# Optimization experiments

Hardware: AMD Instinct MI355X
Metric: run time of the kernel (lower is better)

Reference implementation:

```python
import jax, jax.numpy as jnp
import numpy as np

N, D_IN, D, E, B = 30000, 512, 512, 300000, 4096
N_RES, N_DNN = 2, 2
EPS = 1e-5


def _ln(x, g, b):
    mu = jnp.mean(x, axis=-1, keepdims=True)
    var = jnp.mean((x - mu) ** 2, axis=-1, keepdims=True)
    return (x - mu) * jax.lax.rsqrt(var + EPS) * g + b


def setup_inputs() -> dict:
    key = jax.random.key(0)
    ks = jax.random.split(key, 16)
    s = 1.0 / np.sqrt(D)
    inp = {
        "node_feat": jax.random.normal(ks[0], (N, D_IN), jnp.float32),
        "edge_hop0": jax.random.randint(ks[1], (2, E), 0, N, jnp.int32),
        "edge_hop1": jax.random.randint(ks[2], (2, E), 0, N, jnp.int32),
        "target_idx": jax.random.randint(ks[3], (B,), 0, N, jnp.int32),
        # node transform
        "Wt": jax.random.normal(ks[4], (D_IN, D), jnp.float32) / np.sqrt(D_IN),
        "bt": jnp.zeros((D,), jnp.float32),
        # GATConv (shared across both hops, one relation)
        "Wf": jax.random.normal(ks[5], (D, D), jnp.float32) * s,
        "bf": jnp.zeros((D,), jnp.float32),
        "w_att": jax.random.normal(ks[6], (2 * D,), jnp.float32) * s,
        "b_att": jnp.zeros((), jnp.float32),
        "gat_bias": jnp.zeros((D,), jnp.float32),
        # Res_DNN
        "Wp": jax.random.normal(ks[7], (D, D), jnp.float32) * s,
        "bp": jnp.zeros((D,), jnp.float32),
        "dnn_W": jax.random.normal(ks[8], (N_RES, N_DNN, D, D), jnp.float32) * s,
        "dnn_b": jnp.zeros((N_RES, N_DNN, D), jnp.float32),
        "dnn_g": jnp.ones((N_RES, N_DNN, D), jnp.float32),
        "dnn_beta": jnp.zeros((N_RES, N_DNN, D), jnp.float32),
        "res_g": jnp.ones((N_RES, D), jnp.float32),
        "res_beta": jnp.zeros((N_RES, D), jnp.float32),
        "Wc": jax.random.normal(ks[9], (D, 1), jnp.float32) * s,
        "bc": jnp.zeros((1,), jnp.float32),
    }
    return inp


def _gat(feat, edges, Wf, bf, w_att, b_att, gat_bias):
    # dst and src are the same node set / same features here
    h = feat @ Wf + bf                      # [N, D]
    di, si = edges[0], edges[1]             # [E], [E]
    # att(concat(dst_h, src_h)) == dst_h @ w[:D] + src_h @ w[D:] + b
    sd = h @ w_att[:D]                      # [N]
    ss = h @ w_att[D:]                      # [N]
    e = jnp.tanh(sd[di] + ss[si] + b_att)   # [E]
    # sparse softmax per destination row
    m = jax.ops.segment_max(e, di, num_segments=N)
    a = jnp.exp(e - m[di])
    denom = jax.ops.segment_sum(a, di, num_segments=N)
    alpha = a / denom[di]                   # [E]
    # sparse-mm aggregation
    out = jax.ops.segment_sum(alpha[:, None] * h[si], di, num_segments=N)
    return out + gat_bias


def reference(node_feat, edge_hop0, edge_hop1, target_idx, Wt, bt, Wf, bf,
              w_att, b_att, gat_bias, Wp, bp, dnn_W, dnn_b, dnn_g, dnn_beta,
              res_g, res_beta, Wc, bc):
    # node-type feature transform (dropout is identity at inference)
    feat = node_feat @ Wt + bt              # [N, D]
    # hops processed from last to first: hop1 then hop0
    for edges in (edge_hop1, edge_hop0):
        g = _gat(feat, edges, Wf, bf, w_att, b_att, gat_bias)
        feat = (feat + g) * 0.5             # mean of stacked [orig, gat_out]
    h = feat[target_idx]                    # [B, D]
    # Res_DNN head
    h = h @ Wp + bp
    for r in range(N_RES):
        sc = h
        for i in range(N_DNN):
            h = _ln(jnp.tanh(h @ dnn_W[r, i] + dnn_b[r, i]), dnn_g[r, i], dnn_beta[r, i])
        h = _ln(jnp.tanh(sc + h), res_g[r], res_beta[r])
    logits = h @ Wc + bc                    # [B, 1]
    return jax.nn.sigmoid(logits)
```

## Files before the change

### kernel.cpp

```cpp
#include <hip/hip_runtime.h>

#define D 512
typedef unsigned short ushort_t;
typedef __attribute__((ext_vector_type(8))) short bf16x8;
typedef __attribute__((ext_vector_type(4))) short bf16x4;
typedef __attribute__((ext_vector_type(4))) float f32x4;

static __device__ __forceinline__ ushort_t f2bf(float f) {
  unsigned u = __float_as_uint(f);
  u += 0x7fffu + ((u >> 16) & 1u);
  return (ushort_t)(u >> 16);
}
static __device__ __forceinline__ float bf2f(ushort_t h) {
  return __uint_as_float(((unsigned)h) << 16);
}

static __device__ __forceinline__ void gld_lds16(const void* g, void* lds) {
  __builtin_amdgcn_global_load_lds(
      (const __attribute__((address_space(1))) unsigned int*)g,
      (__attribute__((address_space(3))) unsigned int*)lds, 16, 0, 0);
}

__global__ __launch_bounds__(256) void pack_weight(
    const float* __restrict__ W, ushort_t* __restrict__ out, int K, int N, int nmat) {
  int i = blockIdx.x * 256 + threadIdx.x;
  const int per = K * N;
  if (i >= per * nmat) return;
  const int mat = i / per;
  const int r = i - mat * per;
  const int k = r / N, n = r - k * N;
  const int nt = n >> 4, col = n & 15, kt = k >> 5, kg = (k >> 3) & 3, j = k & 7;
  out[(size_t)mat * per + (((size_t)nt * (K >> 5) + kt) << 9) + ((kg << 4) + col) * 8 + j] =
      f2bf(W[(size_t)mat * per + r]);
}

__global__ __launch_bounds__(256) void conv_bf16_pad(
    const float* __restrict__ in, ushort_t* __restrict__ out, int M, int Mp, int K) {
  const size_t i4 = ((size_t)blockIdx.x * 256 + threadIdx.x) * 4;
  if (i4 >= (size_t)Mp * K) return;
  const int row = (int)(i4 / K);
  ushort4 o;
  if (row < M) {
    const float4 v = *reinterpret_cast<const float4*>(&in[i4]);
    o.x = f2bf(v.x); o.y = f2bf(v.y); o.z = f2bf(v.z); o.w = f2bf(v.w);
  } else {
    o.x = o.y = o.z = o.w = 0;
  }
  *reinterpret_cast<ushort4*>(&out[i4]) = o;
}

__global__ __launch_bounds__(512) void gemm_mfma(
    const ushort_t* __restrict__ A, const ushort_t* __restrict__ Bp,
    const float* __restrict__ bias, ushort_t* __restrict__ C16, int N, int K) {
  __shared__ __align__(16) ushort_t As[2][8 * 512];
  __shared__ __align__(16) ushort_t Bs[2][8 * 512];
  const int nwg = gridDim.x;
  const int q = nwg >> 3, rm = nwg & 7;
  const int xcd = blockIdx.x & 7, kk = blockIdx.x >> 3;
  const int lin = (xcd < rm ? xcd * (q + 1) : rm * (q + 1) + (xcd - rm) * q) + kk;
  const int m0 = (lin >> 2) * 128;
  const int n0 = (lin & 3) * 128;
  const int tid = threadIdx.x;
  const int lane = tid & 63;
  const int wid = tid >> 6;
  const int wm = wid >> 1;
  const int wn = wid & 1;
  const int arow = lane & 15;
  const int akoff = (lane >> 4) * 8;
  const int kt32 = K >> 5;
  f32x4 acc[2][4] = {};

  auto stage = [&](int kt, int b) {
    const int k0 = kt * 32;
    gld_lds16(&A[(size_t)(m0 + wid * 16 + arow) * K + k0 + akoff],
              &As[b][wid * 512]);
    gld_lds16(&Bp[(((size_t)(n0 / 16 + wid) * kt32 + kt) << 9) + lane * 8],
              &Bs[b][wid * 512]);
  };

  stage(0, 0);
  __syncthreads();
  int cur = 0;
  for (int t = 0; t < kt32; ++t) {
    if (t + 1 < kt32) stage(t + 1, cur ^ 1);
    bf16x8 af[2], bfr[4];
#pragma unroll
    for (int mi = 0; mi < 2; ++mi)
      af[mi] = *reinterpret_cast<const bf16x8*>(&As[cur][(wm * 2 + mi) * 512 + lane * 8]);
#pragma unroll
    for (int ni = 0; ni < 4; ++ni)
      bfr[ni] = *reinterpret_cast<const bf16x8*>(&Bs[cur][(wn * 4 + ni) * 512 + lane * 8]);
#pragma unroll
    for (int mi = 0; mi < 2; ++mi)
#pragma unroll
      for (int ni = 0; ni < 4; ++ni)
        acc[mi][ni] = __builtin_amdgcn_mfma_f32_16x16x32_bf16(af[mi], bfr[ni], acc[mi][ni], 0, 0, 0);
    __syncthreads();
    cur ^= 1;
  }
#pragma unroll
  for (int mi = 0; mi < 2; ++mi) {
    const int row = m0 + wm * 32 + mi * 16 + ((lane >> 4) << 2);
#pragma unroll
    for (int ni = 0; ni < 4; ++ni) {
      const int col = n0 + wn * 64 + ni * 16 + (lane & 15);
      const float bv = bias[col];
#pragma unroll
      for (int r = 0; r < 4; ++r)
        C16[(size_t)(row + r) * N + col] = f2bf(acc[mi][ni][r] + bv);
    }
  }
}

__global__ __launch_bounds__(256) void rowdot2_w(
    const ushort_t* __restrict__ hb, const float* __restrict__ w_att,
    float* __restrict__ sd, float* __restrict__ ss, int Nn) {
  const int r = blockIdx.x * 4 + (threadIdx.x >> 6);
  const int lane = threadIdx.x & 63;
  if (r >= Nn) return;
  const bf16x8 hv = *reinterpret_cast<const bf16x8*>(&hb[(size_t)r * D + lane * 8]);
  float d0 = 0.f, d1 = 0.f;
#pragma unroll
  for (int q = 0; q < 8; ++q) {
    const float v = bf2f((ushort_t)hv[q]);
    d0 += v * w_att[lane * 8 + q];
    d1 += v * w_att[D + lane * 8 + q];
  }
#pragma unroll
  for (int off = 32; off > 0; off >>= 1) {
    d0 += __shfl_xor(d0, off);
    d1 += __shfl_xor(d1, off);
  }
  if (lane == 0) { sd[r] = d0; ss[r] = d1; }
}

__global__ void fill_bucket(const int* __restrict__ e1, const int* __restrict__ e0,
                            int* __restrict__ cnt, int* __restrict__ bucket,
                            int Nn, int E) {
  const int e = blockIdx.x * blockDim.x + threadIdx.x;
  if (e >= E) return;
  const int d1 = e1[e];
  const int p1 = atomicAdd(&cnt[d1], 1);
  if (p1 < 64) bucket[(size_t)d1 * 64 + p1] = e1[E + e];
  const int d0 = e0[e];
  const int p0 = atomicAdd(&cnt[Nn + d0], 1);
  if (p0 < 64) bucket[((size_t)(Nn + d0)) * 64 + p0] = e0[E + e];
}

__global__ __launch_bounds__(256) void gat_aggregate_w(
    ushort_t* __restrict__ featb, const ushort_t* __restrict__ hb,
    const float* __restrict__ sd, const float* __restrict__ ss,
    const int* __restrict__ di, const int* __restrict__ si,
    const float* __restrict__ b_att_p, const float* __restrict__ gat_bias,
    const int* __restrict__ cnt, const int* __restrict__ bucket, int Nn, int E) {
  const int wave = threadIdx.x >> 6;
  const int dst = blockIdx.x * 2 + (wave >> 1);
  const int lane = threadIdx.x & 63;
  if (dst >= Nn) return;
  const int colb = (wave & 1) * 256 + lane * 4;
  const int deg = cnt[dst];
  const float sdd = sd[dst];
  const float ba = b_att_p[0];
  const size_t o = (size_t)dst * D + colb;
  bf16x4 fv = *reinterpret_cast<const bf16x4*>(&featb[o]);
  float acc[4] = {};
  if (deg <= 64) {
    const bool valid = lane < deg;
    const int slane = valid ? bucket[(size_t)dst * 64 + lane] : 0;
    const float e = valid ? tanhf(sdd + ss[slane] + ba) : -1e30f;
    float m = e;
#pragma unroll
    for (int off = 32; off > 0; off >>= 1) m = fmaxf(m, __shfl_xor(m, off));
    const float a = valid ? expf(e - m) : 0.f;
    float s = a;
#pragma unroll
    for (int off = 32; off > 0; off >>= 1) s += __shfl_xor(s, off);
    const float w = a * ((s > 0.f) ? 1.f / s : 0.f);
    int k = 0;
    for (; k + 3 < deg; k += 4) {
      const float w0 = __shfl(w, k), w1 = __shfl(w, k + 1);
      const float w2 = __shfl(w, k + 2), w3 = __shfl(w, k + 3);
      const int s0 = __shfl(slane, k), s1 = __shfl(slane, k + 1);
      const int s2 = __shfl(slane, k + 2), s3 = __shfl(slane, k + 3);
      const bf16x4 h0 = *reinterpret_cast<const bf16x4*>(&hb[(size_t)s0 * D + colb]);
      const bf16x4 h1 = *reinterpret_cast<const bf16x4*>(&hb[(size_t)s1 * D + colb]);
      const bf16x4 h2 = *reinterpret_cast<const bf16x4*>(&hb[(size_t)s2 * D + colb]);
      const bf16x4 h3 = *reinterpret_cast<const bf16x4*>(&hb[(size_t)s3 * D + colb]);
#pragma unroll
      for (int qq = 0; qq < 4; ++qq) {
        const float t0 = w0 * bf2f((ushort_t)h0[qq]) + w1 * bf2f((ushort_t)h1[qq]);
        const float t1 = w2 * bf2f((ushort_t)h2[qq]) + w3 * bf2f((ushort_t)h3[qq]);
        acc[qq] += t0 + t1;
      }
    }
    for (; k < deg; ++k) {
      const float wk = __shfl(w, k);
      const int sk = __shfl(slane, k);
      const bf16x4 h0 = *reinterpret_cast<const bf16x4*>(&hb[(size_t)sk * D + colb]);
#pragma unroll
      for (int qq = 0; qq < 4; ++qq) acc[qq] += wk * bf2f((ushort_t)h0[qq]);
    }
  } else {
    float m = -1e30f;
    for (int e = lane; e < E; e += 64)
      if (di[e] == dst) m = fmaxf(m, tanhf(sdd + ss[si[e]] + ba));
#pragma unroll
    for (int off = 32; off > 0; off >>= 1) m = fmaxf(m, __shfl_xor(m, off));
    float s = 0.f;
    for (int e = lane; e < E; e += 64)
      if (di[e] == dst) s += expf(tanhf(sdd + ss[si[e]] + ba) - m);
#pragma unroll
    for (int off = 32; off > 0; off >>= 1) s += __shfl_xor(s, off);
    const float inv = (s > 0.f) ? 1.f / s : 0.f;
    for (int base = 0; base < E; base += 64) {
      const int e = base + lane;
      const bool hit = (e < E) && (di[e] == dst);
      unsigned long long mask = __ballot(hit);
      const int sidx = hit ? si[e] : 0;
      const float aval = hit ? expf(tanhf(sdd + ss[sidx] + ba) - m) * inv : 0.f;
      while (mask) {
        const int l = __ffsll((long long)mask) - 1;
        mask &= mask - 1;
        const float wv = __shfl(aval, l);
        const int sk = __shfl(sidx, l);
        const bf16x4 hv = *reinterpret_cast<const bf16x4*>(&hb[(size_t)sk * D + colb]);
#pragma unroll
        for (int qq = 0; qq < 4; ++qq) acc[qq] += wv * bf2f((ushort_t)hv[qq]);
      }
    }
  }
#pragma unroll
  for (int q = 0; q < 4; ++q) {
    const float f = (bf2f((ushort_t)fv[q]) + acc[q] + gat_bias[colb + q]) * 0.5f;
    fv[q] = (short)f2bf(f);
  }
  *reinterpret_cast<bf16x4*>(&featb[o]) = fv;
}

__global__ __launch_bounds__(1024, 4) void head_fused(
    const ushort_t* __restrict__ featb, const int* __restrict__ tidx,
    const ushort_t* __restrict__ pWp, const float* __restrict__ bp,
    const ushort_t* __restrict__ pDW, const float* __restrict__ dnn_b,
    const float* __restrict__ dnn_g, const float* __restrict__ dnn_be,
    const float* __restrict__ res_g, const float* __restrict__ res_be,
    const float* __restrict__ Wc, const float* __restrict__ bc,
    float* __restrict__ out) {
  __shared__ __align__(16) ushort_t A_lds[16 * 512];
  __shared__ float lsum[16][16], lsq[16][16], meanv[16], rsv[16];
  const int tid = threadIdx.x;
  const int lane = tid & 63;
  const int wave = tid >> 6;
  const int nt0 = wave * 2;
  const int c15 = lane & 15;
  const int rgrp = lane >> 4;

  {
    const int row = tid >> 6, col8 = tid & 63;
    const int g = tidx[blockIdx.x * 16 + row];
    const bf16x8 v = *reinterpret_cast<const bf16x8*>(&featb[(size_t)g * D + col8 * 8]);
    *reinterpret_cast<bf16x8*>(&A_lds[row * 512 + (col8 ^ (row & 7)) * 8]) = v;
  }
  __syncthreads();

  auto do_gemm = [&](const ushort_t* __restrict__ W, f32x4& a0, f32x4& a1) {
    a0 = f32x4{0.f, 0.f, 0.f, 0.f};
    a1 = f32x4{0.f, 0.f, 0.f, 0.f};
    bf16x8 c0 = *reinterpret_cast<const bf16x8*>(
        &W[(((size_t)nt0 * 16 + 0) << 9) + lane * 8]);
    bf16x8 c1 = *reinterpret_cast<const bf16x8*>(
        &W[(((size_t)(nt0 + 1) * 16 + 0) << 9) + lane * 8]);
#pragma unroll
    for (int kt = 0; kt < 16; ++kt) {
      bf16x8 n0 = c0, n1 = c1;
      if (kt < 15) {
        n0 = *reinterpret_cast<const bf16x8*>(
            &W[(((size_t)nt0 * 16 + kt + 1) << 9) + lane * 8]);
        n1 = *reinterpret_cast<const bf16x8*>(
            &W[(((size_t)(nt0 + 1) * 16 + kt + 1) << 9) + lane * 8]);
      }
      const int col8 = kt * 4 + rgrp;
      const bf16x8 af = *reinterpret_cast<const bf16x8*>(
          &A_lds[c15 * 512 + (col8 ^ (c15 & 7)) * 8]);
      a0 = __builtin_amdgcn_mfma_f32_16x16x32_bf16(af, c0, a0, 0, 0, 0);
      a1 = __builtin_amdgcn_mfma_f32_16x16x32_bf16(af, c1, a1, 0, 0, 0);
      c0 = n0;
      c1 = n1;
    }
  };

  auto block_ln = [&](f32x4& v0, f32x4& v1, const float* __restrict__ g,
                      const float* __restrict__ be) {
    float psum[4], psq[4];
#pragma unroll
    for (int r = 0; r < 4; ++r) {
      psum[r] = v0[r] + v1[r];
      psq[r] = v0[r] * v0[r] + v1[r] * v1[r];
    }
#pragma unroll
    for (int off = 8; off > 0; off >>= 1)
#pragma unroll
      for (int r = 0; r < 4; ++r) {
        psum[r] += __shfl_xor(psum[r], off);
        psq[r] += __shfl_xor(psq[r], off);
      }
    if (c15 == 0) {
#pragma unroll
      for (int r = 0; r < 4; ++r) {
        lsum[wave][rgrp * 4 + r] = psum[r];
        lsq[wave][rgrp * 4 + r] = psq[r];
      }
    }
    __syncthreads();
    if (tid < 16) {
      float s = 0.f, qq = 0.f;
#pragma unroll
      for (int w = 0; w < 16; ++w) { s += lsum[w][tid]; qq += lsq[w][tid]; }
      const float mean = s * (1.f / 512.f);
      const float var = qq * (1.f / 512.f) - mean * mean;
      meanv[tid] = mean;
      rsv[tid] = rsqrtf(var + 1e-5f);
    }
    __syncthreads();
    const int col0 = nt0 * 16 + c15;
    const int col1 = (nt0 + 1) * 16 + c15;
    const float g0 = g[col0], b0 = be[col0];
    const float g1 = g[col1], b1 = be[col1];
#pragma unroll
    for (int r = 0; r < 4; ++r) {
      const int row = rgrp * 4 + r;
      v0[r] = (v0[r] - meanv[row]) * rsv[row] * g0 + b0;
      v1[r] = (v1[r] - meanv[row]) * rsv[row] * g1 + b1;
    }
  };

  auto store_A = [&](const f32x4& v0, const f32x4& v1) {
    const int col0 = nt0 * 16 + c15;
    const int col1 = (nt0 + 1) * 16 + c15;
#pragma unroll
    for (int r = 0; r < 4; ++r) {
      const int row = rgrp * 4 + r;
      A_lds[row * 512 + (((col0 >> 3) ^ (row & 7)) << 3) + (col0 & 7)] = f2bf(v0[r]);
      A_lds[row * 512 + (((col1 >> 3) ^ (row & 7)) << 3) + (col1 & 7)] = f2bf(v1[r]);
    }
  };

  f32x4 sc0, sc1, acc0, acc1, ln0, ln1;

  do_gemm(pWp, acc0, acc1);
  {
    const float bv0 = bp[nt0 * 16 + c15];
    const float bv1 = bp[(nt0 + 1) * 16 + c15];
#pragma unroll
    for (int r = 0; r < 4; ++r) { sc0[r] = acc0[r] + bv0; sc1[r] = acc1[r] + bv1; }
  }
  __syncthreads();
  store_A(sc0, sc1);
  __syncthreads();

  for (int rb = 0; rb < 2; ++rb) {
    {
      const int st = rb * 2;
      do_gemm(pDW + (size_t)st * D * D, acc0, acc1);
      const float bv0 = dnn_b[st * D + nt0 * 16 + c15];
      const float bv1 = dnn_b[st * D + (nt0 + 1) * 16 + c15];
#pragma unroll
      for (int r = 0; r < 4; ++r) {
        acc0[r] = tanhf(acc0[r] + bv0);
        acc1[r] = tanhf(acc1[r] + bv1);
      }
      block_ln(acc0, acc1, dnn_g + st * D, dnn_be + st * D);
      store_A(acc0, acc1);
      __syncthreads();
    }
    {
      const int st = rb * 2 + 1;
      do_gemm(pDW + (size_t)st * D * D, ln0, ln1);
      const float bv0 = dnn_b[st * D + nt0 * 16 + c15];
      const float bv1 = dnn_b[st * D + (nt0 + 1) * 16 + c15];
#pragma unroll
      for (int r = 0; r < 4; ++r) {
        ln0[r] = tanhf(ln0[r] + bv0);
        ln1[r] = tanhf(ln1[r] + bv1);
      }
      block_ln(ln0, ln1, dnn_g + st * D, dnn_be + st * D);
    }
#pragma unroll
    for (int r = 0; r < 4; ++r) {
      acc0[r] = tanhf(sc0[r] + ln0[r]);
      acc1[r] = tanhf(sc1[r] + ln1[r]);
    }
    block_ln(acc0, acc1, res_g + rb * D, res_be + rb * D);
    sc0 = acc0;
    sc1 = acc1;
    if (rb == 0) {
      store_A(sc0, sc1);
      __syncthreads();
    }
  }

  float pr[4];
  {
    const float w0 = Wc[nt0 * 16 + c15];
    const float w1 = Wc[(nt0 + 1) * 16 + c15];
#pragma unroll
    for (int r = 0; r < 4; ++r) pr[r] = sc0[r] * w0 + sc1[r] * w1;
  }
#pragma unroll
  for (int off = 8; off > 0; off >>= 1)
#pragma unroll
    for (int r = 0; r < 4; ++r) pr[r] += __shfl_xor(pr[r], off);
  __syncthreads();
  if (c15 == 0) {
#pragma unroll
    for (int r = 0; r < 4; ++r) lsum[wave][rgrp * 4 + r] = pr[r];
  }
  __syncthreads();
  if (tid < 16) {
    float s = 0.f;
#pragma unroll
    for (int w = 0; w < 16; ++w) s += lsum[w][tid];
    out[blockIdx.x * 16 + tid] = 1.f / (1.f + expf(-(s + bc[0])));
  }
}

extern "C" void kernel_launch(void* const* d_in, const int* in_sizes, int n_in,
                              void* d_out, int out_size, void* d_ws, size_t ws_size,
                              hipStream_t stream) {
  (void)n_in; (void)out_size; (void)ws_size;
  const float* node_feat = (const float*)d_in[0];
  const int* edge0 = (const int*)d_in[1];
  const int* edge1 = (const int*)d_in[2];
  const int* tidx = (const int*)d_in[3];
  const float* Wt = (const float*)d_in[4];
  const float* bt = (const float*)d_in[5];
  const float* Wf = (const float*)d_in[6];
  const float* bfp = (const float*)d_in[7];
  const float* w_att = (const float*)d_in[8];
  const float* b_att = (const float*)d_in[9];
  const float* gat_bias = (const float*)d_in[10];
  const float* Wp = (const float*)d_in[11];
  const float* bp = (const float*)d_in[12];
  const float* dnn_W = (const float*)d_in[13];
  const float* dnn_b = (const float*)d_in[14];
  const float* dnn_g = (const float*)d_in[15];
  const float* dnn_be = (const float*)d_in[16];
  const float* res_g = (const float*)d_in[17];
  const float* res_be = (const float*)d_in[18];
  const float* Wc = (const float*)d_in[19];
  const float* bc = (const float*)d_in[20];
  float* out = (float*)d_out;

  const int Nn = in_sizes[0] / D;
  const int E = in_sizes[1] / 2;
  const int B = in_sizes[3];
  const int K_IN = in_sizes[4] / D;
  const int Mp = (Nn + 127) / 128 * 128;
  const int N2 = 2 * Nn;

  char* p = (char*)d_ws;
  auto alloc = [&](size_t bytes) -> char* {
    char* r = p;
    p += (bytes + 255) & ~(size_t)255;
    return r;
  };
  ushort_t* featb = (ushort_t*)alloc((size_t)Mp * D * 2);
  ushort_t* hb = (ushort_t*)alloc((size_t)Mp * D * 2);
  float* sd = (float*)alloc((size_t)Nn * 4);
  float* ss = (float*)alloc((size_t)Nn * 4);
  int* cnt = (int*)alloc((size_t)N2 * 4);
  int* bucket = (int*)alloc((size_t)N2 * 64 * 4);
  ushort_t* pWt = (ushort_t*)alloc((size_t)K_IN * D * 2);
  ushort_t* pWf = (ushort_t*)alloc((size_t)D * D * 2);
  ushort_t* pWp = (ushort_t*)alloc((size_t)D * D * 2);
  ushort_t* pDWall = (ushort_t*)alloc((size_t)4 * D * D * 2);

  dim3 blk(256);
  const int nw2 = (Nn + 1) / 2;

  {
    pack_weight<<<(K_IN * D + 255) / 256, blk, 0, stream>>>(Wt, pWt, K_IN, D, 1);
    pack_weight<<<(D * D + 255) / 256, blk, 0, stream>>>(Wf, pWf, D, D, 1);
    pack_weight<<<(D * D + 255) / 256, blk, 0, stream>>>(Wp, pWp, D, D, 1);
    pack_weight<<<(4 * D * D + 255) / 256, blk, 0, stream>>>(dnn_W, pDWall, D, D, 4);
    conv_bf16_pad<<<((size_t)Mp * K_IN / 4 + 255) / 256, blk, 0, stream>>>(
        node_feat, hb , Nn, Mp, K_IN);
  }

  hipMemsetAsync(cnt, 0, (size_t)N2 * 4, stream);
  fill_bucket<<<(E + 255) / 256, blk, 0, stream>>>(edge1, edge0, cnt, bucket, Nn, E);

  gemm_mfma<<<dim3(4 * (Mp / 128)), dim3(512), 0, stream>>>(hb, pWt, bt, featb, D, K_IN);

  const int* hops[2] = {edge1, edge0};
  for (int hp = 0; hp < 2; ++hp) {
    gemm_mfma<<<dim3(4 * (Mp / 128)), dim3(512), 0, stream>>>(featb, pWf, bfp, hb, D, D);
    rowdot2_w<<<(Nn + 3) / 4, blk, 0, stream>>>(hb, w_att, sd, ss, Nn);
    gat_aggregate_w<<<nw2, blk, 0, stream>>>(
        featb, hb, sd, ss, hops[hp], hops[hp] + E, b_att, gat_bias,
        cnt + hp * Nn, bucket + (size_t)hp * Nn * 64, Nn, E);
  }

  head_fused<<<B / 16, dim3(1024), 0, stream>>>(
      featb, tidx, pWp, bp, pDWall, dnn_b, dnn_g, dnn_be, res_g, res_be,
      Wc, bc, out);
}
```

Baseline: 340.2 us.

## Fuse attention dot products into GEMM epilogue and widen aggregation to one wave per node

The GEMM epilogue now computes partial attention dot products (sd, ss) per 64-column band and writes them to partial buffers. A small combine kernel sums the eight bands, which replaces the separate rowdot2 pass that re-read the whole h matrix. Separately, the GAT aggregation now gives each destination node a single wave that loads 8 bf16 per lane instead of two waves loading 4 each, halving per-node softmax redundancy and widening gathers. The cost is extra epilogue work and partial-buffer traffic. The dot products now use fp32 values before bf16 rounding, which slightly changes numerics.

```diff
diff --git a/kernel.cpp b/kernel.cpp
--- a/kernel.cpp
+++ b/kernel.cpp
@@ -3,7 +3,6 @@
 #define D 512
 typedef unsigned short ushort_t;
 typedef __attribute__((ext_vector_type(8))) short bf16x8;
-typedef __attribute__((ext_vector_type(4))) short bf16x4;
 typedef __attribute__((ext_vector_type(4))) float f32x4;
 
 static __device__ __forceinline__ ushort_t f2bf(float f) {
@@ -51,7 +50,9 @@
 
 __global__ __launch_bounds__(512) void gemm_mfma(
     const ushort_t* __restrict__ A, const ushort_t* __restrict__ Bp,
-    const float* __restrict__ bias, ushort_t* __restrict__ C16, int N, int K) {
+    const float* __restrict__ bias, ushort_t* __restrict__ C16,
+    const float* __restrict__ watt, float* __restrict__ sd_part,
+    float* __restrict__ ss_part, int Mp, int N, int K) {
   __shared__ __align__(16) ushort_t As[2][8 * 512];
   __shared__ __align__(16) ushort_t Bs[2][8 * 512];
   const int nwg = gridDim.x;
@@ -67,6 +68,8 @@
   const int wn = wid & 1;
   const int arow = lane & 15;
   const int akoff = (lane >> 4) * 8;
+  const int c15 = lane & 15;
+  const int rgrp = lane >> 4;
   const int kt32 = K >> 5;
   f32x4 acc[2][4] = {};
 
@@ -98,40 +101,51 @@
     __syncthreads();
     cur ^= 1;
   }
+  const int band = (n0 >> 6) + wn;
 #pragma unroll
   for (int mi = 0; mi < 2; ++mi) {
-    const int row = m0 + wm * 32 + mi * 16 + ((lane >> 4) << 2);
-#pragma unroll
-    for (int ni = 0; ni < 4; ++ni) {
-      const int col = n0 + wn * 64 + ni * 16 + (lane & 15);
-      const float bv = bias[col];
-#pragma unroll
-      for (int r = 0; r < 4; ++r)
-        C16[(size_t)(row + r) * N + col] = f2bf(acc[mi][ni][r] + bv);
-    }
-  }
-}
-
-__global__ __launch_bounds__(256) void rowdot2_w(
-    const ushort_t* __restrict__ hb, const float* __restrict__ w_att,
-    float* __restrict__ sd, float* __restrict__ ss, int Nn) {
-  const int r = blockIdx.x * 4 + (threadIdx.x >> 6);
-  const int lane = threadIdx.x & 63;
-  if (r >= Nn) return;
-  const bf16x8 hv = *reinterpret_cast<const bf16x8*>(&hb[(size_t)r * D + lane * 8]);
-  float d0 = 0.f, d1 = 0.f;
-#pragma unroll
-  for (int q = 0; q < 8; ++q) {
-    const float v = bf2f((ushort_t)hv[q]);
-    d0 += v * w_att[lane * 8 + q];
-    d1 += v * w_att[D + lane * 8 + q];
-  }
-#pragma unroll
-  for (int off = 32; off > 0; off >>= 1) {
-    d0 += __shfl_xor(d0, off);
-    d1 += __shfl_xor(d1, off);
-  }
-  if (lane == 0) { sd[r] = d0; ss[r] = d1; }
+    const int row = m0 + wm * 32 + mi * 16 + (rgrp << 2);
+#pragma unroll
+    for (int r = 0; r < 4; ++r) {
+      float psd = 0.f, pss = 0.f;
+#pragma unroll
+      for (int ni = 0; ni < 4; ++ni) {
+        const int col = n0 + wn * 64 + ni * 16 + c15;
+        const float v = acc[mi][ni][r] + bias[col];
+        C16[(size_t)(row + r) * N + col] = f2bf(v);
+        if (watt) {
+          psd += v * watt[col];
+          pss += v * watt[D + col];
+        }
+      }
+      if (watt) {
+#pragma unroll
+        for (int off = 8; off > 0; off >>= 1) {
+          psd += __shfl_xor(psd, off);
+          pss += __shfl_xor(pss, off);
+        }
+        if (c15 == 0) {
+          sd_part[(size_t)band * Mp + row + r] = psd;
+          ss_part[(size_t)band * Mp + row + r] = pss;
+        }
+      }
+    }
+  }
+}
+
+__global__ __launch_bounds__(256) void combine_dots(
+    const float* __restrict__ sd_part, const float* __restrict__ ss_part,
+    float* __restrict__ sd, float* __restrict__ ss, int Mp, int Nn) {
+  const int i = blockIdx.x * 256 + threadIdx.x;
+  if (i >= Nn) return;
+  float a = 0.f, b = 0.f;
+#pragma unroll
+  for (int bnd = 0; bnd < 8; ++bnd) {
+    a += sd_part[(size_t)bnd * Mp + i];
+    b += ss_part[(size_t)bnd * Mp + i];
+  }
+  sd[i] = a;
+  ss[i] = b;
 }
 
 __global__ void fill_bucket(const int* __restrict__ e1, const int* __restrict__ e0,
@@ -153,17 +167,15 @@
     const int* __restrict__ di, const int* __restrict__ si,
     const float* __restrict__ b_att_p, const float* __restrict__ gat_bias,
     const int* __restrict__ cnt, const int* __restrict__ bucket, int Nn, int E) {
-  const int wave = threadIdx.x >> 6;
-  const int dst = blockIdx.x * 2 + (wave >> 1);
+  const int dst = blockIdx.x * 4 + (threadIdx.x >> 6);
   const int lane = threadIdx.x & 63;
   if (dst >= Nn) return;
-  const int colb = (wave & 1) * 256 + lane * 4;
   const int deg = cnt[dst];
   const float sdd = sd[dst];
   const float ba = b_att_p[0];
-  const size_t o = (size_t)dst * D + colb;
-  bf16x4 fv = *reinterpret_cast<const bf16x4*>(&featb[o]);
-  float acc[4] = {};
+  const size_t o = (size_t)dst * D + lane * 8;
+  bf16x8 fv = *reinterpret_cast<const bf16x8*>(&featb[o]);
+  float acc[8] = {};
   if (deg <= 64) {
     const bool valid = lane < deg;
     const int slane = valid ? bucket[(size_t)dst * 64 + lane] : 0;
@@ -182,12 +194,12 @@
       const float w2 = __shfl(w, k + 2), w3 = __shfl(w, k + 3);
       const int s0 = __shfl(slane, k), s1 = __shfl(slane, k + 1);
       const int s2 = __shfl(slane, k + 2), s3 = __shfl(slane, k + 3);
-      const bf16x4 h0 = *reinterpret_cast<const bf16x4*>(&hb[(size_t)s0 * D + colb]);
-      const bf16x4 h1 = *reinterpret_cast<const bf16x4*>(&hb[(size_t)s1 * D + colb]);
-      const bf16x4 h2 = *reinterpret_cast<const bf16x4*>(&hb[(size_t)s2 * D + colb]);
-      const bf16x4 h3 = *reinterpret_cast<const bf16x4*>(&hb[(size_t)s3 * D + colb]);
-#pragma unroll
-      for (int qq = 0; qq < 4; ++qq) {
+      const bf16x8 h0 = *reinterpret_cast<const bf16x8*>(&hb[(size_t)s0 * D + lane * 8]);
+      const bf16x8 h1 = *reinterpret_cast<const bf16x8*>(&hb[(size_t)s1 * D + lane * 8]);
+      const bf16x8 h2 = *reinterpret_cast<const bf16x8*>(&hb[(size_t)s2 * D + lane * 8]);
+      const bf16x8 h3 = *reinterpret_cast<const bf16x8*>(&hb[(size_t)s3 * D + lane * 8]);
+#pragma unroll
+      for (int qq = 0; qq < 8; ++qq) {
         const float t0 = w0 * bf2f((ushort_t)h0[qq]) + w1 * bf2f((ushort_t)h1[qq]);
         const float t1 = w2 * bf2f((ushort_t)h2[qq]) + w3 * bf2f((ushort_t)h3[qq]);
         acc[qq] += t0 + t1;
@@ -196,9 +208,9 @@
     for (; k < deg; ++k) {
       const float wk = __shfl(w, k);
       const int sk = __shfl(slane, k);
-      const bf16x4 h0 = *reinterpret_cast<const bf16x4*>(&hb[(size_t)sk * D + colb]);
-#pragma unroll
-      for (int qq = 0; qq < 4; ++qq) acc[qq] += wk * bf2f((ushort_t)h0[qq]);
+      const bf16x8 h0 = *reinterpret_cast<const bf16x8*>(&hb[(size_t)sk * D + lane * 8]);
+#pragma unroll
+      for (int qq = 0; qq < 8; ++qq) acc[qq] += wk * bf2f((ushort_t)h0[qq]);
     }
   } else {
     float m = -1e30f;
@@ -223,18 +235,18 @@
         mask &= mask - 1;
         const float wv = __shfl(aval, l);
         const int sk = __shfl(sidx, l);
-        const bf16x4 hv = *reinterpret_cast<const bf16x4*>(&hb[(size_t)sk * D + colb]);
-#pragma unroll
-        for (int qq = 0; qq < 4; ++qq) acc[qq] += wv * bf2f((ushort_t)hv[qq]);
-      }
-    }
-  }
-#pragma unroll
-  for (int q = 0; q < 4; ++q) {
-    const float f = (bf2f((ushort_t)fv[q]) + acc[q] + gat_bias[colb + q]) * 0.5f;
+        const bf16x8 hv = *reinterpret_cast<const bf16x8*>(&hb[(size_t)sk * D + lane * 8]);
+#pragma unroll
+        for (int qq = 0; qq < 8; ++qq) acc[qq] += wv * bf2f((ushort_t)hv[qq]);
+      }
+    }
+  }
+#pragma unroll
+  for (int q = 0; q < 8; ++q) {
+    const float f = (bf2f((ushort_t)fv[q]) + acc[q] + gat_bias[lane * 8 + q]) * 0.5f;
     fv[q] = (short)f2bf(f);
   }
-  *reinterpret_cast<bf16x4*>(&featb[o]) = fv;
+  *reinterpret_cast<bf16x8*>(&featb[o]) = fv;
 }
 
 __global__ __launch_bounds__(1024, 4) void head_fused(
@@ -467,6 +479,8 @@
   ushort_t* hb = (ushort_t*)alloc((size_t)Mp * D * 2);
   float* sd = (float*)alloc((size_t)Nn * 4);
   float* ss = (float*)alloc((size_t)Nn * 4);
+  float* sd_part = (float*)alloc((size_t)8 * Mp * 4);
+  float* ss_part = (float*)alloc((size_t)8 * Mp * 4);
   int* cnt = (int*)alloc((size_t)N2 * 4);
   int* bucket = (int*)alloc((size_t)N2 * 64 * 4);
   ushort_t* pWt = (ushort_t*)alloc((size_t)K_IN * D * 2);
@@ -475,7 +489,7 @@
   ushort_t* pDWall = (ushort_t*)alloc((size_t)4 * D * D * 2);
 
   dim3 blk(256);
-  const int nw2 = (Nn + 1) / 2;
+  const int nw4 = (Nn + 3) / 4;
 
   {
     pack_weight<<<(K_IN * D + 255) / 256, blk, 0, stream>>>(Wt, pWt, K_IN, D, 1);
@@ -489,13 +503,15 @@
   hipMemsetAsync(cnt, 0, (size_t)N2 * 4, stream);
   fill_bucket<<<(E + 255) / 256, blk, 0, stream>>>(edge1, edge0, cnt, bucket, Nn, E);
 
-  gemm_mfma<<<dim3(4 * (Mp / 128)), dim3(512), 0, stream>>>(hb, pWt, bt, featb, D, K_IN);
+  gemm_mfma<<<dim3(4 * (Mp / 128)), dim3(512), 0, stream>>>(
+      hb, pWt, bt, featb, nullptr, nullptr, nullptr, Mp, D, K_IN);
 
   const int* hops[2] = {edge1, edge0};
   for (int hp = 0; hp < 2; ++hp) {
-    gemm_mfma<<<dim3(4 * (Mp / 128)), dim3(512), 0, stream>>>(featb, pWf, bfp, hb, D, D);
-    rowdot2_w<<<(Nn + 3) / 4, blk, 0, stream>>>(hb, w_att, sd, ss, Nn);
-    gat_aggregate_w<<<nw2, blk, 0, stream>>>(
+    gemm_mfma<<<dim3(4 * (Mp / 128)), dim3(512), 0, stream>>>(
+        featb, pWf, bfp, hb, w_att, sd_part, ss_part, Mp, D, D);
+    combine_dots<<<(Nn + 255) / 256, blk, 0, stream>>>(sd_part, ss_part, sd, ss, Mp, Nn);
+    gat_aggregate_w<<<nw4, blk, 0, stream>>>(
         featb, hb, sd, ss, hops[hp], hops[hp] + E, b_att, gat_bias,
         cnt + hp * Nn, bucket + (size_t)hp * Nn * 64, Nn, E);
   }
```

After: 342.9 us. Within noise of the previous version (+0.8%).
